# Optimization experiments

Measured on AMD Instinct MI355X. Metric: run time of the kernel, lower is better.

## Reference

```python
import jax, jax.numpy as jnp
import numpy as np
import math

B, L, E, H = 512, 200, 64, 4
D = E // H
NEG = jnp.float32(-(2.0 ** 32) + 1.0)


def setup_inputs() -> dict:
    key = jax.random.key(0)
    ks = jax.random.split(key, 12)
    inp = jax.random.normal(ks[0], (B, L, E), dtype=jnp.float32)
    # realistic variable-length histories: mask[b, t] = t < len_b, len_b in [1, L]
    lens = jax.random.randint(ks[1], (B, 1), 1, L + 1)
    mask = jnp.arange(L)[None, :] < lens  # [B, L] bool
    s = 1.0 / math.sqrt(E)
    pos_enc = jax.random.normal(ks[2], (1, L, E), dtype=jnp.float32)
    Wk = jax.random.uniform(ks[3], (E, E), jnp.float32, -s, s)
    bk = jnp.zeros((E,), jnp.float32)
    Wv = jax.random.uniform(ks[4], (E, E), jnp.float32, -s, s)
    bv = jnp.zeros((E,), jnp.float32)
    Wq = jax.random.uniform(ks[5], (E, E), jnp.float32, -s, s)
    bq = jnp.zeros((E,), jnp.float32)
    Wf = jax.random.uniform(ks[6], (E, E), jnp.float32, -s, s)
    bf = jnp.zeros((E,), jnp.float32)
    return {"input": inp, "mask": mask, "pos_enc": pos_enc,
            "Wk": Wk, "bk": bk, "Wv": Wv, "bv": bv,
            "Wq": Wq, "bq": bq, "Wf": Wf, "bf": bf}


def reference(input, mask, pos_enc, Wk, bk, Wv, bv, Wq, bq, Wf, bf):
    x = input + pos_enc  # [B, L, E]
    # project and split heads: [B, H, L, D]
    def split(t):
        return t.reshape(B, L, H, D).transpose(0, 2, 1, 3)
    k = split(x @ Wk.T + bk)
    v = split(x @ Wv.T + bv)
    q = split(x @ Wq.T + bq) / math.sqrt(D)
    scores = jnp.einsum('bhqd,bhkd->bhqk', q, k)  # [B, H, L, L]
    # key_mask in torch code broadcasts over dim 3 (mask on the QUERY axis),
    # query_mask is its transpose (mask on the KEY axis). Combined: both must be valid.
    both = mask[:, None, :, None] & mask[:, None, None, :]  # [B, 1, L, L]
    scores = jnp.where(both, scores, NEG)
    attn = jax.nn.softmax(scores, axis=-1)
    # dropout is identity at inference; omitted deterministically
    out = jnp.einsum('bhqk,bhkd->bhqd', attn, v)
    out = out.transpose(0, 2, 1, 3).reshape(B, L, E)
    out = out @ Wf.T + bf
    fm = mask.astype(jnp.float32)[:, :, None]  # [B, L, 1]
    lens = jnp.sum(fm, axis=1)  # [B, 1]
    pooled = jnp.sum(out * fm, axis=1) / (lens + 1e-8)  # [B, E]
    return pooled
```

## Files before the change

### kernel.cpp

```cpp
#include <hip/hip_runtime.h>
#include <hip/hip_fp16.h>
#include <math.h>

#define Bn 512
#define Ln 200
#define En 64
#define Hn 4
#define Dn 16
#define KS3 18
#define VS3 200
#define QSC 0.36067376022224085f

typedef _Float16 __f16;
typedef __f16 f16x4 __attribute__((ext_vector_type(4)));
typedef __f16 f16x8 __attribute__((ext_vector_type(8)));
typedef float f32x4 __attribute__((ext_vector_type(4)));

#if __has_builtin(__builtin_amdgcn_exp2f)
__device__ __forceinline__ float fexp2(float x) { return __builtin_amdgcn_exp2f(x); }
#else
__device__ __forceinline__ float fexp2(float x) { return exp2f(x); }
#endif

__device__ __forceinline__ f16x8 pack8s(float4 a, float4 b, float4 pa, float4 pb) {
    f16x8 r;
    r[0] = (__f16)(a.x + pa.x); r[1] = (__f16)(a.y + pa.y);
    r[2] = (__f16)(a.z + pa.z); r[3] = (__f16)(a.w + pa.w);
    r[4] = (__f16)(b.x + pb.x); r[5] = (__f16)(b.y + pb.y);
    r[6] = (__f16)(b.z + pb.z); r[7] = (__f16)(b.w + pb.w);
    return r;
}
__device__ __forceinline__ f16x8 pack8(float4 a, float4 b) {
    f16x8 r;
    r[0] = (__f16)a.x; r[1] = (__f16)a.y; r[2] = (__f16)a.z; r[3] = (__f16)a.w;
    r[4] = (__f16)b.x; r[5] = (__f16)b.y; r[6] = (__f16)b.z; r[7] = (__f16)b.w;
    return r;
}

__global__ __launch_bounds__(256, 4) void fused_kernel(
    const float* __restrict__ input, const int* __restrict__ mask,
    const float* __restrict__ pos_enc,
    const float* __restrict__ Wk, const float* __restrict__ bk,
    const float* __restrict__ Wv, const float* __restrict__ bv,
    const float* __restrict__ Wq, const float* __restrict__ bq,
    const float* __restrict__ Wf, const float* __restrict__ bf_,
    float* __restrict__ out)
{
    __shared__ __align__(16) __f16 Kh[Ln * KS3];
    __shared__ __align__(16) __f16 Qh[Ln * KS3];
    __shared__ __align__(16) __f16 Vt[16 * VS3];
    __shared__ float lred[4][4][16];
    __shared__ float red[4][16];
    __shared__ float ph[16];
    __shared__ int cnt_red[4];

    const int tid  = threadIdx.x;
    const int b    = blockIdx.x >> 2, h = blockIdx.x & 3;
    const int wave = tid >> 6, lane = tid & 63;
    const int quad = lane >> 4, ln16 = lane & 15;

    const int mv = (tid < Ln) ? mask[b * Ln + tid] : 0;

    f16x8 bfr[3][2];
    #pragma unroll
    for (int m = 0; m < 3; ++m) {
        const float* W = (m == 0) ? Wk : (m == 1) ? Wv : Wq;
        #pragma unroll
        for (int ks = 0; ks < 2; ++ks) {
            const float4* wp = (const float4*)(W + (size_t)(h * 16 + ln16) * 64) + (ks * 8 + quad * 2);
            bfr[m][ks] = pack8(wp[0], wp[1]);
        }
    }
    const int cg = h * 16 + ln16;
    const float bkv = bk[cg], bvv = bv[cg], bqv = bq[cg];

    int c = (mv != 0) ? 1 : 0;
    #pragma unroll
    for (int off = 32; off; off >>= 1) c += __shfl_down(c, off, 64);
    if (lane == 0) cnt_red[wave] = c;
    __syncthreads();
    const int len = cnt_red[0] + cnt_red[1] + cnt_red[2] + cnt_red[3];
    const int nt = (len + 15) >> 4;

    const float4* in4 = (const float4*)(input + (size_t)b * Ln * En);
    const float4* pe4 = (const float4*)pos_enc;

    for (int rt = wave; rt < nt; rt += 4) {
        const int R = rt * 16 + ln16;
        const bool rok = (R < Ln);
        f16x8 af[2];
        #pragma unroll
        for (int ks = 0; ks < 2; ++ks) {
            float4 xa = {0,0,0,0}, xb = {0,0,0,0}, pa = {0,0,0,0}, pb = {0,0,0,0};
            if (rok) {
                const int o4 = R * 16 + ks * 8 + quad * 2;
                xa = in4[o4]; xb = in4[o4 + 1];
                pa = pe4[o4]; pb = pe4[o4 + 1];
            }
            af[ks] = pack8s(xa, xb, pa, pb);
        }
        f32x4 acc[3];
        #pragma unroll
        for (int m = 0; m < 3; ++m) acc[m] = (f32x4){0,0,0,0};
        #pragma unroll
        for (int ks = 0; ks < 2; ++ks)
            #pragma unroll
            for (int m = 0; m < 3; ++m)
                acc[m] = __builtin_amdgcn_mfma_f32_16x16x32_f16(af[ks], bfr[m][ks], acc[m], 0, 0, 0);

        #pragma unroll
        for (int j = 0; j < 4; ++j) {
            const int t = rt * 16 + quad * 4 + j;
            if (t < Ln) {
                Kh[t * KS3 + ln16] = (__f16)(acc[0][j] + bkv);
                Qh[t * KS3 + ln16] = (__f16)((acc[2][j] + bqv) * QSC);
            }
        }
        const int vc0 = rt * 16 + quad * 4;
        if (vc0 < Ln) {
            f16x4 vp;
            #pragma unroll
            for (int j = 0; j < 4; ++j) vp[j] = (__f16)(acc[1][j] + bvv);
            *(f16x4*)(Vt + ln16 * VS3 + vc0) = vp;
        }
    }
    __syncthreads();

    const int nquad = (nt + 3) >> 2;
    int g, kh, nkh;
    if (nquad >= 3)      { g = wave;     kh = 0;         nkh = 1; }
    else if (nquad == 2) { g = wave & 1; kh = wave >> 1; nkh = 2; }
    else                 { g = 0;        kh = wave;      nkh = 4; }
    const bool active = (g < nquad);
    const int nktp = (nt + nkh - 1) / nkh;
    const int klo = kh * nktp;
    const int khi = min(klo + nktp, nt);
    const int qt0 = 4 * g;

    const f16x4 ones = {(__f16)1.f, (__f16)1.f, (__f16)1.f, (__f16)1.f};
    f32x4 o2[4], lacc[4];
    #pragma unroll
    for (int i = 0; i < 4; ++i) { o2[i] = (f32x4){0,0,0,0}; lacc[i] = (f32x4){0,0,0,0}; }

    if (active && klo < khi) {
        f16x4 qf[4];
        #pragma unroll
        for (int i = 0; i < 4; ++i) {
            int qr = min((qt0 + i) * 16 + ln16, Ln - 1);
            qf[i] = *(const f16x4*)(Qh + qr * KS3 + quad * 4);
        }
        const bool needmask = (khi == nt);
        const int kfull = khi - (needmask ? 1 : 0);

        f16x4 kf = *(const f16x4*)(Kh + min(klo * 16 + ln16, Ln - 1) * KS3 + quad * 4);
        f16x4 vf = *(const f16x4*)(Vt + ln16 * VS3 + min(klo * 16 + quad * 4, Ln - 4));

        for (int kt = klo; kt < kfull; ++kt) {
            const int krn = min((kt + 1) * 16 + ln16, Ln - 1);
            const int vcn = min((kt + 1) * 16 + quad * 4, Ln - 4);
            const f16x4 kfn = *(const f16x4*)(Kh + krn * KS3 + quad * 4);
            const f16x4 vfn = *(const f16x4*)(Vt + ln16 * VS3 + vcn);
            f32x4 s[4];
            #pragma unroll
            for (int i = 0; i < 4; ++i)
                s[i] = __builtin_amdgcn_mfma_f32_16x16x16f16(kf, qf[i], (f32x4){0,0,0,0}, 0, 0, 0);
            f16x4 pf[4];
            #pragma unroll
            for (int i = 0; i < 4; ++i) {
                #pragma unroll
                for (int j = 0; j < 4; ++j)
                    pf[i][j] = (__f16)fexp2(fminf(s[i][j], 14.5f));
            }
            #pragma unroll
            for (int i = 0; i < 4; ++i) {
                o2[i]   = __builtin_amdgcn_mfma_f32_16x16x16f16(vf,   pf[i], o2[i],   0, 0, 0);
                lacc[i] = __builtin_amdgcn_mfma_f32_16x16x16f16(ones, pf[i], lacc[i], 0, 0, 0);
            }
            kf = kfn; vf = vfn;
        }
        if (needmask) {
            const int kbase = (nt - 1) * 16 + quad * 4;
            f32x4 s[4];
            #pragma unroll
            for (int i = 0; i < 4; ++i)
                s[i] = __builtin_amdgcn_mfma_f32_16x16x16f16(kf, qf[i], (f32x4){0,0,0,0}, 0, 0, 0);
            f16x4 pf[4];
            #pragma unroll
            for (int i = 0; i < 4; ++i) {
                #pragma unroll
                for (int j = 0; j < 4; ++j) {
                    const bool kok = (kbase + j) < len;
                    pf[i][j] = kok ? (__f16)fexp2(fminf(s[i][j], 14.5f)) : (__f16)0.f;
                }
            }
            #pragma unroll
            for (int i = 0; i < 4; ++i) {
                o2[i]   = __builtin_amdgcn_mfma_f32_16x16x16f16(vf,   pf[i], o2[i],   0, 0, 0);
                lacc[i] = __builtin_amdgcn_mfma_f32_16x16x16f16(ones, pf[i], lacc[i], 0, 0, 0);
            }
        }
    }

    float l[4];
    #pragma unroll
    for (int i = 0; i < 4; ++i) l[i] = lacc[i][0];

    if (nkh > 1) {
        if (lane < 16) {
            #pragma unroll
            for (int i = 0; i < 4; ++i) lred[wave][i][lane] = l[i];
        }
        __syncthreads();
        #pragma unroll
        for (int i = 0; i < 4; ++i) {
            if (nkh == 2) l[i] = lred[g][i][ln16] + lred[g + 2][i][ln16];
            else          l[i] = lred[0][i][ln16] + lred[1][i][ln16]
                               + lred[2][i][ln16] + lred[3][i][ln16];
        }
    }

    f32x4 pool = {0.f, 0.f, 0.f, 0.f};
    if (active) {
        #pragma unroll
        for (int i = 0; i < 4; ++i) {
            const float rs = ((qt0 + i) * 16 + ln16 < len) ? 1.f / l[i] : 0.f;
            #pragma unroll
            for (int j = 0; j < 4; ++j) pool[j] = fmaf(o2[i][j], rs, pool[j]);
        }
    }

    #pragma unroll
    for (int j = 0; j < 4; ++j) {
        #pragma unroll
        for (int off = 1; off < 16; off <<= 1) pool[j] += __shfl_xor(pool[j], off, 64);
    }
    if (ln16 == 0) {
        #pragma unroll
        for (int j = 0; j < 4; ++j) red[wave][quad * 4 + j] = pool[j];
    }
    __syncthreads();
    if (tid < 16)
        ph[tid] = (red[0][tid] + red[1][tid] + red[2][tid] + red[3][tid]) / ((float)len + 1e-8f);
    __syncthreads();

    if (tid < 64) {
        const int e = tid;
        const float* wr = Wf + (size_t)e * 64 + h * 16;
        float a = (h == 0) ? bf_[e] : 0.f;
        #pragma unroll
        for (int i = 0; i < 16; ++i) a = fmaf(wr[i], ph[i], a);
        atomicAdd(out + b * En + e, a);
    }
}

extern "C" void kernel_launch(void* const* d_in, const int* in_sizes, int n_in,
                              void* d_out, int out_size, void* d_ws, size_t ws_size,
                              hipStream_t stream) {
    const float* input   = (const float*)d_in[0];
    const int*   mask    = (const int*)  d_in[1];
    const float* pos_enc = (const float*)d_in[2];
    const float* Wk      = (const float*)d_in[3];
    const float* bk      = (const float*)d_in[4];
    const float* Wv      = (const float*)d_in[5];
    const float* bv      = (const float*)d_in[6];
    const float* Wq      = (const float*)d_in[7];
    const float* bq      = (const float*)d_in[8];
    const float* Wf      = (const float*)d_in[9];
    const float* bf      = (const float*)d_in[10];

    float* out = (float*)d_out;
    hipMemsetAsync(out, 0, (size_t)Bn * En * sizeof(float), stream);

    fused_kernel<<<Bn * Hn, 256, 0, stream>>>(input, mask, pos_enc,
                                              Wk, bk, Wv, bv, Wq, bq, Wf, bf, out);
}
```

Measured before the change: 122.7 us.

## Template attention core on active query tiles, use packed RTZ converts and setprio

The attention inner loop moves into a template specialized on the number of live query tiles (1-4), picked through a wave-uniform switch. This skips the MFMA and exp work a wave would otherwise spend on padded query tiles beyond the sequence length. It also packs the fp16 probabilities with cvt_pkrtz, which uses round-toward-zero instead of the default rounding, and wraps the MFMA groups in s_setprio. The cost is four instantiations of the loop, which enlarge the code and may raise register pressure, plus a small change in rounding.

```diff
diff --git a/kernel.cpp b/kernel.cpp
--- a/kernel.cpp
+++ b/kernel.cpp
@@ -12,6 +12,7 @@
 #define QSC 0.36067376022224085f
 
 typedef _Float16 __f16;
+typedef __fp16 fp16x2 __attribute__((ext_vector_type(2)));
 typedef __f16 f16x4 __attribute__((ext_vector_type(4)));
 typedef __f16 f16x8 __attribute__((ext_vector_type(8)));
 typedef float f32x4 __attribute__((ext_vector_type(4)));
@@ -35,6 +36,91 @@
     r[0] = (__f16)a.x; r[1] = (__f16)a.y; r[2] = (__f16)a.z; r[3] = (__f16)a.w;
     r[4] = (__f16)b.x; r[5] = (__f16)b.y; r[6] = (__f16)b.z; r[7] = (__f16)b.w;
     return r;
+}
+
+__device__ __forceinline__ f16x4 pack4rtz(float e0, float e1, float e2, float e3) {
+    const fp16x2 lo = __builtin_amdgcn_cvt_pkrtz(e0, e1);
+    const fp16x2 hi = __builtin_amdgcn_cvt_pkrtz(e2, e3);
+    f16x4 r;
+    r[0] = (__f16)lo[0]; r[1] = (__f16)lo[1];
+    r[2] = (__f16)hi[0]; r[3] = (__f16)hi[1];
+    return r;
+}
+
+template<int NI>
+__device__ __forceinline__ void attn_core(
+    const __f16* __restrict__ Kh_, const __f16* __restrict__ Qh_, const __f16* __restrict__ Vt_,
+    int qt0, int klo, int khi, int nt, int len, int quad, int ln16,
+    f32x4 (&o2)[4], f32x4 (&lacc)[4])
+{
+    const f16x4 ones = {(__f16)1.f, (__f16)1.f, (__f16)1.f, (__f16)1.f};
+    f16x4 qf[NI];
+    #pragma unroll
+    for (int i = 0; i < NI; ++i) {
+        int qr = min((qt0 + i) * 16 + ln16, Ln - 1);
+        qf[i] = *(const f16x4*)(Qh_ + qr * KS3 + quad * 4);
+    }
+    const bool needmask = (khi == nt);
+    const int kfull = khi - (needmask ? 1 : 0);
+
+    f16x4 kf = *(const f16x4*)(Kh_ + min(klo * 16 + ln16, Ln - 1) * KS3 + quad * 4);
+    f16x4 vf = *(const f16x4*)(Vt_ + ln16 * VS3 + min(klo * 16 + quad * 4, Ln - 4));
+
+    for (int kt = klo; kt < kfull; ++kt) {
+        const int krn = min((kt + 1) * 16 + ln16, Ln - 1);
+        const int vcn = min((kt + 1) * 16 + quad * 4, Ln - 4);
+        const f16x4 kfn = *(const f16x4*)(Kh_ + krn * KS3 + quad * 4);
+        const f16x4 vfn = *(const f16x4*)(Vt_ + ln16 * VS3 + vcn);
+        f32x4 s[NI];
+        __builtin_amdgcn_s_setprio(1);
+        #pragma unroll
+        for (int i = 0; i < NI; ++i)
+            s[i] = __builtin_amdgcn_mfma_f32_16x16x16f16(kf, qf[i], (f32x4){0,0,0,0}, 0, 0, 0);
+        __builtin_amdgcn_s_setprio(0);
+        f16x4 pf[NI];
+        #pragma unroll
+        for (int i = 0; i < NI; ++i) {
+            pf[i] = pack4rtz(fexp2(fminf(s[i][0], 14.5f)),
+                             fexp2(fminf(s[i][1], 14.5f)),
+                             fexp2(fminf(s[i][2], 14.5f)),
+                             fexp2(fminf(s[i][3], 14.5f)));
+        }
+        __builtin_amdgcn_s_setprio(1);
+        #pragma unroll
+        for (int i = 0; i < NI; ++i) {
+            o2[i]   = __builtin_amdgcn_mfma_f32_16x16x16f16(vf,   pf[i], o2[i],   0, 0, 0);
+            lacc[i] = __builtin_amdgcn_mfma_f32_16x16x16f16(ones, pf[i], lacc[i], 0, 0, 0);
+        }
+        __builtin_amdgcn_s_setprio(0);
+        kf = kfn; vf = vfn;
+    }
+    if (needmask) {
+        const int kbase = (nt - 1) * 16 + quad * 4;
+        f32x4 s[NI];
+        __builtin_amdgcn_s_setprio(1);
+        #pragma unroll
+        for (int i = 0; i < NI; ++i)
+            s[i] = __builtin_amdgcn_mfma_f32_16x16x16f16(kf, qf[i], (f32x4){0,0,0,0}, 0, 0, 0);
+        __builtin_amdgcn_s_setprio(0);
+        f16x4 pf[NI];
+        #pragma unroll
+        for (int i = 0; i < NI; ++i) {
+            float e[4];
+            #pragma unroll
+            for (int j = 0; j < 4; ++j) {
+                const bool kok = (kbase + j) < len;
+                e[j] = kok ? fexp2(fminf(s[i][j], 14.5f)) : 0.f;
+            }
+            pf[i] = pack4rtz(e[0], e[1], e[2], e[3]);
+        }
+        __builtin_amdgcn_s_setprio(1);
+        #pragma unroll
+        for (int i = 0; i < NI; ++i) {
+            o2[i]   = __builtin_amdgcn_mfma_f32_16x16x16f16(vf,   pf[i], o2[i],   0, 0, 0);
+            lacc[i] = __builtin_amdgcn_mfma_f32_16x16x16f16(ones, pf[i], lacc[i], 0, 0, 0);
+        }
+        __builtin_amdgcn_s_setprio(0);
+    }
 }
 
 __global__ __launch_bounds__(256, 4) void fused_kernel(
@@ -137,67 +223,17 @@
     const int khi = min(klo + nktp, nt);
     const int qt0 = 4 * g;
 
-    const f16x4 ones = {(__f16)1.f, (__f16)1.f, (__f16)1.f, (__f16)1.f};
     f32x4 o2[4], lacc[4];
     #pragma unroll
     for (int i = 0; i < 4; ++i) { o2[i] = (f32x4){0,0,0,0}; lacc[i] = (f32x4){0,0,0,0}; }
 
     if (active && klo < khi) {
-        f16x4 qf[4];
-        #pragma unroll
-        for (int i = 0; i < 4; ++i) {
-            int qr = min((qt0 + i) * 16 + ln16, Ln - 1);
-            qf[i] = *(const f16x4*)(Qh + qr * KS3 + quad * 4);
-        }
-        const bool needmask = (khi == nt);
-        const int kfull = khi - (needmask ? 1 : 0);
-
-        f16x4 kf = *(const f16x4*)(Kh + min(klo * 16 + ln16, Ln - 1) * KS3 + quad * 4);
-        f16x4 vf = *(const f16x4*)(Vt + ln16 * VS3 + min(klo * 16 + quad * 4, Ln - 4));
-
-        for (int kt = klo; kt < kfull; ++kt) {
-            const int krn = min((kt + 1) * 16 + ln16, Ln - 1);
-            const int vcn = min((kt + 1) * 16 + quad * 4, Ln - 4);
-            const f16x4 kfn = *(const f16x4*)(Kh + krn * KS3 + quad * 4);
-            const f16x4 vfn = *(const f16x4*)(Vt + ln16 * VS3 + vcn);
-            f32x4 s[4];
-            #pragma unroll
-            for (int i = 0; i < 4; ++i)
-                s[i] = __builtin_amdgcn_mfma_f32_16x16x16f16(kf, qf[i], (f32x4){0,0,0,0}, 0, 0, 0);
-            f16x4 pf[4];
-            #pragma unroll
-            for (int i = 0; i < 4; ++i) {
-                #pragma unroll
-                for (int j = 0; j < 4; ++j)
-                    pf[i][j] = (__f16)fexp2(fminf(s[i][j], 14.5f));
-            }
-            #pragma unroll
-            for (int i = 0; i < 4; ++i) {
-                o2[i]   = __builtin_amdgcn_mfma_f32_16x16x16f16(vf,   pf[i], o2[i],   0, 0, 0);
-                lacc[i] = __builtin_amdgcn_mfma_f32_16x16x16f16(ones, pf[i], lacc[i], 0, 0, 0);
-            }
-            kf = kfn; vf = vfn;
-        }
-        if (needmask) {
-            const int kbase = (nt - 1) * 16 + quad * 4;
-            f32x4 s[4];
-            #pragma unroll
-            for (int i = 0; i < 4; ++i)
-                s[i] = __builtin_amdgcn_mfma_f32_16x16x16f16(kf, qf[i], (f32x4){0,0,0,0}, 0, 0, 0);
-            f16x4 pf[4];
-            #pragma unroll
-            for (int i = 0; i < 4; ++i) {
-                #pragma unroll
-                for (int j = 0; j < 4; ++j) {
-                    const bool kok = (kbase + j) < len;
-                    pf[i][j] = kok ? (__f16)fexp2(fminf(s[i][j], 14.5f)) : (__f16)0.f;
-                }
-            }
-            #pragma unroll
-            for (int i = 0; i < 4; ++i) {
-                o2[i]   = __builtin_amdgcn_mfma_f32_16x16x16f16(vf,   pf[i], o2[i],   0, 0, 0);
-                lacc[i] = __builtin_amdgcn_mfma_f32_16x16x16f16(ones, pf[i], lacc[i], 0, 0, 0);
-            }
+        const int ni = __builtin_amdgcn_readfirstlane(min(4, nt - qt0));
+        switch (ni) {
+            case 1:  attn_core<1>(Kh, Qh, Vt, qt0, klo, khi, nt, len, quad, ln16, o2, lacc); break;
+            case 2:  attn_core<2>(Kh, Qh, Vt, qt0, klo, khi, nt, len, quad, ln16, o2, lacc); break;
+            case 3:  attn_core<3>(Kh, Qh, Vt, qt0, klo, khi, nt, len, quad, ln16, o2, lacc); break;
+            default: attn_core<4>(Kh, Qh, Vt, qt0, klo, khi, nt, len, quad, ln16, o2, lacc); break;
         }
     }
 
```

Result: no change. 124.3 us (+1.3%).
